# Performance work log

Hardware: AMD Instinct MI355X
Metric: run time of the kernel (lower is better)

The kernel has to match this reference:

```python
import jax, jax.numpy as jnp
import numpy as np

N, E, G = 50000, 800000, 512
DIN, H, DOUT, L = 128, 256, 128, 5
H4 = 4 * H


def _ffnn(h, W1, b1, W2, b2):
    # Linear -> exact GELU (torch default) -> Linear
    return jax.nn.gelu(h @ W1 + b1, approximate=False) @ W2 + b2


def _mean_pool(h, batch):
    s = jax.ops.segment_sum(h, batch, num_segments=G)
    c = jax.ops.segment_sum(jnp.ones((h.shape[0], 1), h.dtype), batch, num_segments=G)
    return s / jnp.maximum(c, 1.0)


def setup_inputs() -> dict:
    key = jax.random.key(0)
    ks = iter(jax.random.split(key, 64))
    w = lambda *s: jax.random.normal(next(ks), s, jnp.float32) * 0.02
    z = lambda *s: jnp.zeros(s, jnp.float32)
    inp = {
        'x': jax.random.normal(next(ks), (N, DIN), jnp.float32),
        'edge_index': jax.random.randint(next(ks), (2, E), 0, N, jnp.int32),
        'batch': jnp.sort(jax.random.randint(next(ks), (N,), 0, G, jnp.int32)),
        'pre_W1': w(DIN, H), 'pre_b1': z(H), 'pre_W2': w(H, H), 'pre_b2': z(H),
        'gin_W1': w(L, H, H), 'gin_b1': z(L, H), 'gin_W2': w(L, H, H), 'gin_b2': z(L, H),
        'ffn_W1': w(L, H, H), 'ffn_b1': z(L, H), 'ffn_W2': w(L, H, H), 'ffn_b2': z(L, H),
        'upd_W1': w(L, H, H), 'upd_b1': z(L, H), 'upd_W2': w(L, H, H4), 'upd_b2': z(L, H4),
        'prop_W1': w(L, H4, H), 'prop_b1': z(L, H), 'prop_W2': w(L, H, H), 'prop_b2': z(L, H),
        'bn_gamma': jnp.ones((L, H), jnp.float32), 'bn_beta': z(L, H),
        'vn': jax.random.normal(next(ks), (1, H4), jnp.float32),
        'post_W1': w(H, H), 'post_b1': z(H), 'post_W2': w(H, DOUT), 'post_b2': z(DOUT),
    }
    return inp


def reference(x, edge_index, batch,
              pre_W1, pre_b1, pre_W2, pre_b2,
              gin_W1, gin_b1, gin_W2, gin_b2,
              ffn_W1, ffn_b1, ffn_W2, ffn_b2,
              upd_W1, upd_b1, upd_W2, upd_b2,
              prop_W1, prop_b1, prop_W2, prop_b2,
              bn_gamma, bn_beta, vn,
              post_W1, post_b1, post_W2, post_b2):
    src, dst = edge_index[0], edge_index[1]
    h = _ffnn(x, pre_W1, pre_b1, pre_W2, pre_b2)
    for i in range(L):
        # virtual node update and propagation
        v = vn + _ffnn(_mean_pool(h, batch), upd_W1[i], upd_b1[i], upd_W2[i], upd_b2[i])  # [G, 4H]
        outvn = _ffnn(v, prop_W1[i], prop_b1[i], prop_W2[i], prop_b2[i])  # [G, H]
        # GINConv (eps=0): nn((1+eps)*h + sum_{j->i} h_j), residual
        agg = jax.ops.segment_sum(h[src], dst, num_segments=N)
        h = _ffnn(h + agg, gin_W1[i], gin_b1[i], gin_W2[i], gin_b2[i]) + h
        # BatchNorm1d (batch statistics, biased var)
        mu = jnp.mean(h, axis=0)
        var = jnp.mean((h - mu) ** 2, axis=0)
        h = (h - mu) * jax.lax.rsqrt(var + 1e-5) * bn_gamma[i] + bn_beta[i]
        # broadcast VN to nodes, FFNN with residual (dropout = identity in eval)
        h = _ffnn(outvn[batch] + h, ffn_W1[i], ffn_b1[i], ffn_W2[i], ffn_b2[i]) + h
    out = _ffnn(_mean_pool(h, batch), post_W1, post_b1, post_W2, post_b2)
    return out
```

## Files before the change

### kernel.cpp

```cpp
#include <hip/hip_runtime.h>
#include <hip/hip_bf16.h>
#include <math.h>

#define NN 50000
#define NNP 50048
#define NE 800000
#define NG 512
#define DIN 128
#define HD 256
#define DOUT 128
#define NL 5
#define H4 1024

typedef _Float16 f16x8 __attribute__((ext_vector_type(8)));
typedef _Float16 f16x4 __attribute__((ext_vector_type(4)));
typedef float f32x4 __attribute__((ext_vector_type(4)));

__device__ __forceinline__ float gelu_exact(float x) {
    return 0.5f * x * (1.0f + erff(x * 0.70710678118654752f));
}

__device__ __forceinline__ void gl_lds16(const _Float16* g, _Float16* l) {
    __builtin_amdgcn_global_load_lds(
        (const __attribute__((address_space(1))) unsigned int*)g,
        (__attribute__((address_space(3))) unsigned int*)l, 16, 0, 0);
}

__global__ void k_hist(const int* __restrict__ idx, int* __restrict__ cnt, int n) {
    int i = blockIdx.x * blockDim.x + threadIdx.x;
    if (i < n) atomicAdd(&cnt[idx[i]], 1);
}

__global__ void k_scan_small(const int* __restrict__ in, int* __restrict__ out, int n) {
    __shared__ int buf[1024];
    int t = threadIdx.x;
    int v = (t < n) ? in[t] : 0;
    buf[t] = v;
    __syncthreads();
    for (int off = 1; off < 1024; off <<= 1) {
        int x = (t >= off) ? buf[t - off] : 0;
        __syncthreads();
        buf[t] += x;
        __syncthreads();
    }
    if (t < n) out[t] = buf[t] - v;
    if (t == 1023) out[n] = buf[1023];
}

__global__ void k_scan_part(const int* __restrict__ in, int* __restrict__ bsum, int n) {
    __shared__ int buf[256];
    int i = blockIdx.x * 256 + threadIdx.x;
    buf[threadIdx.x] = (i < n) ? in[i] : 0;
    __syncthreads();
    for (int off = 128; off > 0; off >>= 1) {
        if (threadIdx.x < off) buf[threadIdx.x] += buf[threadIdx.x + off];
        __syncthreads();
    }
    if (threadIdx.x == 0) bsum[blockIdx.x] = buf[0];
}

__global__ void k_scan_mid(const int* __restrict__ bsum, int* __restrict__ bexcl, int nb,
                           int* __restrict__ out, int n) {
    __shared__ int buf[1024];
    int t = threadIdx.x;
    int v = (t < nb) ? bsum[t] : 0;
    buf[t] = v;
    __syncthreads();
    for (int off = 1; off < 1024; off <<= 1) {
        int x = (t >= off) ? buf[t - off] : 0;
        __syncthreads();
        buf[t] += x;
        __syncthreads();
    }
    if (t < nb) bexcl[t] = buf[t] - v;
    if (t == 1023) out[n] = buf[1023];
}

__global__ void k_scan_out(const int* __restrict__ in, const int* __restrict__ bexcl,
                           int* __restrict__ out, int n) {
    __shared__ int buf[256];
    int i = blockIdx.x * 256 + threadIdx.x;
    int t = threadIdx.x;
    int v = (i < n) ? in[i] : 0;
    buf[t] = v;
    __syncthreads();
    for (int off = 1; off < 256; off <<= 1) {
        int x = (t >= off) ? buf[t - off] : 0;
        __syncthreads();
        buf[t] += x;
        __syncthreads();
    }
    if (i < n) out[i] = bexcl[blockIdx.x] + buf[t] - v;
}

__global__ void k_fill_csr(const int* __restrict__ src, const int* __restrict__ dst,
                           const int* __restrict__ eoff, int* __restrict__ cursor,
                           int* __restrict__ csr, int n) {
    int e = blockIdx.x * blockDim.x + threadIdx.x;
    if (e < n) {
        int d = dst[e];
        int p = atomicAdd(&cursor[d], 1);
        csr[eoff[d] + p] = src[e];
    }
}

__global__ void k_cvt16(const float* __restrict__ in, _Float16* __restrict__ out, int n4) {
    int i = blockIdx.x * blockDim.x + threadIdx.x;
    if (i < n4) {
        float4 v = *(const float4*)&in[i * 4];
        f16x4 o = { (_Float16)v.x, (_Float16)v.y, (_Float16)v.z, (_Float16)v.w };
        *(f16x4*)&out[i * 4] = o;
    }
}

#define NWTJOBS 44
struct WtJobs {
    const float* src[NWTJOBS];
    _Float16* dst[NWTJOBS];
    short K32[NWTJOBS];
    short N32[NWTJOBS];
    short pre[NWTJOBS + 1];
};
__global__ void k_wtb(WtJobs j) {
    int bid = blockIdx.x;
    int lo = 0;
    while (j.pre[lo + 1] <= bid) ++lo;
    int tl = bid - j.pre[lo];
    int nx = j.N32[lo];
    int n0 = (tl % nx) * 32, k0 = (tl / nx) * 32;
    int K = j.K32[lo] * 32, N = nx * 32;
    const float* W = j.src[lo];
    _Float16* Wt = j.dst[lo];
    __shared__ float tile[32][33];
    for (int i = threadIdx.y; i < 32; i += 8)
        tile[i][threadIdx.x] = W[(size_t)(k0 + i) * N + n0 + threadIdx.x];
    __syncthreads();
    for (int i = threadIdx.y; i < 32; i += 8)
        Wt[(size_t)(n0 + i) * K + k0 + threadIdx.x] = (_Float16)tile[threadIdx.x][i];
}

__global__ void k_pool16(const _Float16* __restrict__ h16, const int* __restrict__ goff,
                         _Float16* __restrict__ pool) {
    int g = blockIdx.x;
    int c = threadIdx.x;
    int s = goff[g], e = goff[g + 1];
    float acc = 0.f;
    for (int r = s; r < e; ++r) acc += (float)h16[(size_t)r * HD + c];
    int cnt = e - s;
    pool[g * HD + c] = (_Float16)(acc / (float)(cnt > 0 ? cnt : 1));
}

__global__ __launch_bounds__(256) void k_agg16(const _Float16* __restrict__ h16,
                                               const int* __restrict__ eoff,
                                               const int* __restrict__ csr,
                                               _Float16* __restrict__ out) {
    int node = blockIdx.x * 4 + (threadIdx.x >> 6);
    int lane = threadIdx.x & 63;
    int half = lane >> 5, l = lane & 31;
    f16x8 mine = *(const f16x8*)&h16[(size_t)node * HD + l * 8];
    float acc[8];
#pragma unroll
    for (int q = 0; q < 8; ++q) acc[q] = half ? 0.f : (float)mine[q];
    int s = eoff[node], e = eoff[node + 1];
    for (int base = s; base < e; base += 64) {
        int myi = base + lane;
        int vidx = (myi < e) ? csr[myi] : 0;
        int cnt = min(64, e - base);
        int jj = 0;
        for (; jj + 7 < cnt; jj += 8) {
            int s0 = __shfl(vidx, jj + half);
            int s1 = __shfl(vidx, jj + 2 + half);
            int s2 = __shfl(vidx, jj + 4 + half);
            int s3 = __shfl(vidx, jj + 6 + half);
            f16x8 v0 = *(const f16x8*)&h16[(size_t)s0 * HD + l * 8];
            f16x8 v1 = *(const f16x8*)&h16[(size_t)s1 * HD + l * 8];
            f16x8 v2 = *(const f16x8*)&h16[(size_t)s2 * HD + l * 8];
            f16x8 v3 = *(const f16x8*)&h16[(size_t)s3 * HD + l * 8];
#pragma unroll
            for (int q = 0; q < 8; ++q)
                acc[q] += ((float)v0[q] + (float)v1[q]) + ((float)v2[q] + (float)v3[q]);
        }
        for (; jj + 3 < cnt; jj += 4) {
            int s0 = __shfl(vidx, jj + half);
            int s1 = __shfl(vidx, jj + 2 + half);
            f16x8 v0 = *(const f16x8*)&h16[(size_t)s0 * HD + l * 8];
            f16x8 v1 = *(const f16x8*)&h16[(size_t)s1 * HD + l * 8];
#pragma unroll
            for (int q = 0; q < 8; ++q) acc[q] += (float)v0[q] + (float)v1[q];
        }
        for (; jj < cnt; jj += 2) {
            int i0 = jj + half;
            int s0 = __shfl(vidx, i0);
            if (i0 < cnt) {
                f16x8 v0 = *(const f16x8*)&h16[(size_t)s0 * HD + l * 8];
#pragma unroll
                for (int q = 0; q < 8; ++q) acc[q] += (float)v0[q];
            }
        }
    }
#pragma unroll
    for (int q = 0; q < 8; ++q) acc[q] += __shfl_xor(acc[q], 32);
    if (!half) {
        f16x8 o;
#pragma unroll
        for (int q = 0; q < 8; ++q) o[q] = (_Float16)acc[q];
        *(f16x8*)&out[(size_t)node * HD + l * 8] = o;
    }
}

__global__ void k_bn_final(float* __restrict__ stat,
                           const float* __restrict__ gamma, const float* __restrict__ beta,
                           float* __restrict__ scale, float* __restrict__ shift) {
    int c = threadIdx.x;
    float mu = stat[c] * (1.0f / NN);
    float var = stat[HD + c] * (1.0f / NN) - mu * mu;
    float rs = rsqrtf(var + 1e-5f);
    float sc = rs * gamma[c];
    scale[c] = sc;
    shift[c] = beta[c] - mu * sc;
    stat[c] = 0.f;
    stat[HD + c] = 0.f;
}

template <bool ABN1, bool RES2, bool RESBN2, bool STATS2, int K1>
__global__ __launch_bounds__(512) void k_b2b(const _Float16* __restrict__ A16,
                                             const _Float16* __restrict__ G16,
                                             const _Float16* __restrict__ W1t,
                                             const float* __restrict__ b1,
                                             const _Float16* __restrict__ W2t,
                                             const float* __restrict__ b2,
                                             const _Float16* __restrict__ R16,
                                             const float* __restrict__ bnsc,
                                             const float* __restrict__ bnsh,
                                             const float* __restrict__ ovn,
                                             const int* __restrict__ batchv,
                                             float* __restrict__ stat,
                                             _Float16* __restrict__ C16,
                                             int M) {
    __shared__ _Float16 AC[32][64][8];
    __shared__ _Float16 Bs[3][4][256][8];
    constexpr int NT1 = K1 >> 5;
    constexpr int NSTEP = NT1 + 8;
    const int t = threadIdx.x;
    const int w = t >> 6, lane = t & 63;
    const int m0 = blockIdx.x * 64;
    const int kb = lane >> 4, fr = lane & 15, rr = lane >> 4;

    auto stageB = [&](int s) {
        const _Float16* Wt = (s < NT1) ? W1t : W2t;
        const int KB = (s < NT1) ? K1 : HD;
        const int k0 = ((s < NT1) ? s : (s - NT1)) << 5;
        const int buf = s % 3;
        int s0 = t, s1 = t + 512;
        gl_lds16(Wt + (size_t)(s0 & 255) * KB + k0 + (s0 >> 8) * 8, &Bs[buf][s0 >> 8][s0 & 255][0]);
        gl_lds16(Wt + (size_t)(s1 & 255) * KB + k0 + (s1 >> 8) * 8, &Bs[buf][s1 >> 8][s1 & 255][0]);
    };

    float b1r[2];
#pragma unroll
    for (int ni = 0; ni < 2; ++ni) b1r[ni] = b1[w * 32 + ni * 16 + fr];

    if constexpr (ABN1) {
        for (int c = t; c < K1 * 8; c += 512) {
            int kblk = c >> 6, row = c & 63;
            int b0 = batchv[min(m0 + row, M - 1)];
            const int c0 = kblk * 8;
            f16x8 g = *(const f16x8*)&G16[(size_t)(m0 + row) * HD + c0];
            f16x8 r0;
#pragma unroll
            for (int q = 0; q < 8; ++q)
                r0[q] = (_Float16)((float)g[q] * bnsc[c0 + q] + bnsh[c0 + q] +
                                   ovn[(size_t)b0 * HD + c0 + q]);
            *(f16x8*)&AC[kblk][row][0] = r0;
        }
    } else {
        for (int c = t; c < K1 * 8; c += 512) {
            int kblk = c >> 6, row = c & 63;
            gl_lds16(A16 + (size_t)(m0 + row) * K1 + kblk * 8, &AC[kblk][row][0]);
        }
    }
    stageB(0);
    stageB(1);
    asm volatile("s_waitcnt vmcnt(2) lgkmcnt(0)" ::: "memory");
    __builtin_amdgcn_s_barrier();

    f32x4 acc1[4][2];
#pragma unroll
    for (int mi = 0; mi < 4; ++mi)
#pragma unroll
        for (int ni = 0; ni < 2; ++ni) acc1[mi][ni] = (f32x4){0.f, 0.f, 0.f, 0.f};

#pragma unroll
    for (int s = 0; s < NT1; ++s) {
        if (s) {
            asm volatile("s_waitcnt vmcnt(2)" ::: "memory");
            __builtin_amdgcn_s_barrier();
        }
        f16x8 af[4], bf[2];
#pragma unroll
        for (int mi = 0; mi < 4; ++mi)
            af[mi] = *(const f16x8*)&AC[(s << 2) + kb][mi * 16 + fr][0];
#pragma unroll
        for (int ni = 0; ni < 2; ++ni)
            bf[ni] = *(const f16x8*)&Bs[s % 3][kb][w * 32 + ni * 16 + fr][0];
        stageB(s + 2);
#pragma unroll
        for (int mi = 0; mi < 4; ++mi)
#pragma unroll
            for (int ni = 0; ni < 2; ++ni)
                acc1[mi][ni] = __builtin_amdgcn_mfma_f32_16x16x32_f16(af[mi], bf[ni], acc1[mi][ni], 0, 0, 0);
    }

    asm volatile("s_waitcnt vmcnt(2)" ::: "memory");
    __builtin_amdgcn_s_barrier();
#pragma unroll
    for (int mi = 0; mi < 4; ++mi) {
#pragma unroll
        for (int reg = 0; reg < 4; ++reg) {
            int ml = mi * 16 + rr * 4 + reg;
#pragma unroll
            for (int ni = 0; ni < 2; ++ni) {
                int n = w * 32 + ni * 16 + fr;
                float v = gelu_exact(acc1[mi][ni][reg] + b1r[ni]);
                AC[n >> 3][ml][n & 7] = (_Float16)v;
            }
        }
    }
    asm volatile("s_waitcnt lgkmcnt(0)" ::: "memory");
    __builtin_amdgcn_s_barrier();

    f32x4 acc2[4][2];
#pragma unroll
    for (int mi = 0; mi < 4; ++mi)
#pragma unroll
        for (int ni = 0; ni < 2; ++ni) acc2[mi][ni] = (f32x4){0.f, 0.f, 0.f, 0.f};

#pragma unroll
    for (int s2 = 0; s2 < 8; ++s2) {
        const int s = NT1 + s2;
        if (s2) {
            if (s2 == 7) asm volatile("s_waitcnt vmcnt(0)" ::: "memory");
            else asm volatile("s_waitcnt vmcnt(2)" ::: "memory");
            __builtin_amdgcn_s_barrier();
        }
        f16x8 af[4], bf[2];
#pragma unroll
        for (int mi = 0; mi < 4; ++mi)
            af[mi] = *(const f16x8*)&AC[s2 * 4 + kb][mi * 16 + fr][0];
#pragma unroll
        for (int ni = 0; ni < 2; ++ni)
            bf[ni] = *(const f16x8*)&Bs[s % 3][kb][w * 32 + ni * 16 + fr][0];
        if (s + 2 < NSTEP) stageB(s + 2);
#pragma unroll
        for (int mi = 0; mi < 4; ++mi)
#pragma unroll
            for (int ni = 0; ni < 2; ++ni)
                acc2[mi][ni] = __builtin_amdgcn_mfma_f32_16x16x32_f16(af[mi], bf[ni], acc2[mi][ni], 0, 0, 0);
    }

    float cs[2] = {0.f, 0.f}, cq[2] = {0.f, 0.f};
#pragma unroll
    for (int mi = 0; mi < 4; ++mi) {
#pragma unroll
        for (int reg = 0; reg < 4; ++reg) {
            int m = m0 + mi * 16 + rr * 4 + reg;
            if (m < M) {
#pragma unroll
                for (int ni = 0; ni < 2; ++ni) {
                    int n = w * 32 + ni * 16 + fr;
                    float v = acc2[mi][ni][reg] + b2[n];
                    if (RES2) v += (float)R16[(size_t)m * HD + n];
                    if (RESBN2) v += (float)R16[(size_t)m * HD + n] * bnsc[n] + bnsh[n];
                    _Float16 vh = (_Float16)v;
                    C16[(size_t)m * HD + n] = vh;
                    if (STATS2) { float vr = (float)vh; cs[ni] += vr; cq[ni] += vr * vr; }
                }
            }
        }
    }
    if constexpr (STATS2) {
#pragma unroll
        for (int ni = 0; ni < 2; ++ni) {
            cs[ni] += __shfl_xor(cs[ni], 16); cs[ni] += __shfl_xor(cs[ni], 32);
            cq[ni] += __shfl_xor(cq[ni], 16); cq[ni] += __shfl_xor(cq[ni], 32);
        }
        if (lane < 16) {
#pragma unroll
            for (int ni = 0; ni < 2; ++ni) {
                int n = w * 32 + ni * 16 + lane;
                atomicAdd(&stat[n], cs[ni]);
                atomicAdd(&stat[HD + n], cq[ni]);
            }
        }
    }
}

template <bool GELU, bool BIAS2, bool O32, bool O16>
__global__ __launch_bounds__(256) void k_mgemm(const _Float16* __restrict__ A,
                                               const _Float16* __restrict__ Wt,
                                               const float* __restrict__ bias,
                                               const float* __restrict__ bias2,
                                               float* __restrict__ C32,
                                               _Float16* __restrict__ C16,
                                               int M, int N, int K) {
    __shared__ _Float16 As[2][4][64][8];
    __shared__ _Float16 Bs[2][4][128][8];
    const int t = threadIdx.x;
    const int w = t >> 6, lane = t & 63;
    const int m0 = blockIdx.y * 64, n0 = blockIdx.x * 128;
    const int kb = lane >> 4, fr = lane & 15;

    f32x4 acc[4][2];
#pragma unroll
    for (int mi = 0; mi < 4; ++mi)
#pragma unroll
        for (int ni = 0; ni < 2; ++ni) acc[mi][ni] = (f32x4){0.f, 0.f, 0.f, 0.f};

    const _Float16* gA0 = A + (size_t)(m0 + lane) * K + w * 8;
    const _Float16* gB0 = Wt + (size_t)(n0 + lane) * K + w * 8;
    const _Float16* gB1 = Wt + (size_t)(n0 + 64 + lane) * K + w * 8;

    auto stage = [&](int buf, int k0) {
        gl_lds16(gB0 + k0, &Bs[buf][w][0][0]);
        gl_lds16(gB1 + k0, &Bs[buf][w][64][0]);
        gl_lds16(gA0 + k0, &As[buf][w][0][0]);
    };

    const int nt = K >> 5;
    stage(0, 0);
    __syncthreads();
    for (int tt = 0; tt < nt; ++tt) {
        const int cur = tt & 1;
        if (tt + 1 < nt) stage(cur ^ 1, (tt + 1) << 5);
        f16x8 af[4], bf[2];
#pragma unroll
        for (int mi = 0; mi < 4; ++mi)
            af[mi] = *(const f16x8*)&As[cur][kb][mi * 16 + fr][0];
#pragma unroll
        for (int ni = 0; ni < 2; ++ni)
            bf[ni] = *(const f16x8*)&Bs[cur][kb][w * 32 + ni * 16 + fr][0];
#pragma unroll
        for (int mi = 0; mi < 4; ++mi)
#pragma unroll
            for (int ni = 0; ni < 2; ++ni)
                acc[mi][ni] = __builtin_amdgcn_mfma_f32_16x16x32_f16(af[mi], bf[ni], acc[mi][ni], 0, 0, 0);
        __syncthreads();
    }

    const int rr = lane >> 4;
#pragma unroll
    for (int mi = 0; mi < 4; ++mi) {
#pragma unroll
        for (int reg = 0; reg < 4; ++reg) {
            int m = m0 + mi * 16 + rr * 4 + reg;
            if (m < M) {
#pragma unroll
                for (int ni = 0; ni < 2; ++ni) {
                    int n = n0 + w * 32 + ni * 16 + fr;
                    float v = acc[mi][ni][reg] + bias[n];
                    if (BIAS2) v += bias2[n];
                    if (GELU) v = gelu_exact(v);
                    if (O32) C32[(size_t)m * N + n] = v;
                    if (O16) C16[(size_t)m * N + n] = (_Float16)v;
                }
            }
        }
    }
}

static inline void mg_gelu(hipStream_t st, const _Float16* A, const _Float16* Wt,
                           const float* bias, _Float16* C16, int M, int N, int K) {
    dim3 g(N / 128, (M + 63) / 64), b(256);
    k_mgemm<true, false, false, true><<<g, b, 0, st>>>(A, Wt, bias, nullptr, nullptr, C16, M, N, K);
}
static inline void mg_bias2_16(hipStream_t st, const _Float16* A, const _Float16* Wt,
                               const float* bias, const float* bias2, _Float16* C16,
                               int M, int N, int K) {
    dim3 g(N / 128, (M + 63) / 64), b(256);
    k_mgemm<false, true, false, true><<<g, b, 0, st>>>(A, Wt, bias, bias2, nullptr, C16, M, N, K);
}
static inline void mg_f32only(hipStream_t st, const _Float16* A, const _Float16* Wt,
                              const float* bias, float* C32, int M, int N, int K) {
    dim3 g(N / 128, (M + 63) / 64), b(256);
    k_mgemm<false, false, true, false><<<g, b, 0, st>>>(A, Wt, bias, nullptr, C32, nullptr, M, N, K);
}

extern "C" void kernel_launch(void* const* d_in, const int* in_sizes, int n_in,
                              void* d_out, int out_size, void* d_ws, size_t ws_size,
                              hipStream_t stream) {
    const float* x       = (const float*)d_in[0];
    const int*   ei      = (const int*)d_in[1];
    const int*   batch   = (const int*)d_in[2];
    const float* pre_W1  = (const float*)d_in[3];
    const float* pre_b1  = (const float*)d_in[4];
    const float* pre_W2  = (const float*)d_in[5];
    const float* pre_b2  = (const float*)d_in[6];
    const float* gin_W1  = (const float*)d_in[7];
    const float* gin_b1  = (const float*)d_in[8];
    const float* gin_W2  = (const float*)d_in[9];
    const float* gin_b2  = (const float*)d_in[10];
    const float* ffn_W1  = (const float*)d_in[11];
    const float* ffn_b1  = (const float*)d_in[12];
    const float* ffn_W2  = (const float*)d_in[13];
    const float* ffn_b2  = (const float*)d_in[14];
    const float* upd_W1  = (const float*)d_in[15];
    const float* upd_b1  = (const float*)d_in[16];
    const float* upd_W2  = (const float*)d_in[17];
    const float* upd_b2  = (const float*)d_in[18];
    const float* prop_W1 = (const float*)d_in[19];
    const float* prop_b1 = (const float*)d_in[20];
    const float* prop_W2 = (const float*)d_in[21];
    const float* prop_b2 = (const float*)d_in[22];
    const float* bn_gamma= (const float*)d_in[23];
    const float* bn_beta = (const float*)d_in[24];
    const float* vn      = (const float*)d_in[25];
    const float* post_W1 = (const float*)d_in[26];
    const float* post_b1 = (const float*)d_in[27];
    const float* post_W2 = (const float*)d_in[28];
    const float* post_b2 = (const float*)d_in[29];
    float* out = (float*)d_out;

    const int* e_src = ei;
    const int* e_dst = ei + NE;

    char* p = (char*)d_ws;
    auto alloc = [&](size_t bytes) -> char* {
        char* r = p;
        p += (bytes + 255) & ~(size_t)255;
        return r;
    };
    _Float16* h16    = (_Float16*)alloc((size_t)NNP * HD * 2);
    _Float16* g16    = (_Float16*)alloc((size_t)NNP * HD * 2);
    _Float16* t16a   = (_Float16*)alloc((size_t)NNP * HD * 2);
    _Float16* pool16 = (_Float16*)alloc((size_t)NG * HD * 2);
    _Float16* u16    = (_Float16*)alloc((size_t)NG * HD * 2);
    _Float16* vb16   = (_Float16*)alloc((size_t)NG * H4 * 2);
    _Float16* p16    = (_Float16*)alloc((size_t)NG * HD * 2);
    float*    outvn32= (float*)alloc((size_t)NG * HD * 4);
    float*    bnstat = (float*)alloc(2 * HD * 4);
    float*    bnscale= (float*)alloc(HD * 4);
    float*    bnshift= (float*)alloc(HD * 4);
    _Float16* preW1t = (_Float16*)alloc((size_t)HD * DIN * 2);
    _Float16* preW2t = (_Float16*)alloc((size_t)HD * HD * 2);
    _Float16* ginW1t = (_Float16*)alloc((size_t)NL * HD * HD * 2);
    _Float16* ginW2t = (_Float16*)alloc((size_t)NL * HD * HD * 2);
    _Float16* ffnW1t = (_Float16*)alloc((size_t)NL * HD * HD * 2);
    _Float16* ffnW2t = (_Float16*)alloc((size_t)NL * HD * HD * 2);
    _Float16* updW1t = (_Float16*)alloc((size_t)NL * HD * HD * 2);
    _Float16* updW2t = (_Float16*)alloc((size_t)NL * HD * H4 * 2);
    _Float16* propW1t= (_Float16*)alloc((size_t)NL * H4 * HD * 2);
    _Float16* propW2t= (_Float16*)alloc((size_t)NL * HD * HD * 2);
    _Float16* postW1t= (_Float16*)alloc((size_t)HD * HD * 2);
    _Float16* postW2t= (_Float16*)alloc((size_t)DOUT * HD * 2);
    int* gcount = (int*)alloc(NG * 4);
    int* goff   = (int*)alloc((NG + 1) * 4);
    int* deg    = (int*)alloc(NN * 4);
    int* eoff   = (int*)alloc((NN + 1) * 4);
    int* cursor = (int*)alloc(NN * 4);
    int* csr    = (int*)alloc((size_t)NE * 4);
    int* bsum   = (int*)alloc(1024 * 4);
    int* bexcl  = (int*)alloc(1024 * 4);
    _Float16* x16 = t16a;

    {
        size_t span = (size_t)((char*)(cursor + NN) - (char*)gcount);
        hipMemsetAsync(gcount, 0, span, stream);
        hipMemsetAsync(bnstat, 0, 2 * HD * 4, stream);
    }
    hipLaunchKernelGGL(k_hist, dim3((NN + 255) / 256), dim3(256), 0, stream, batch, gcount, NN);
    hipLaunchKernelGGL(k_hist, dim3((NE + 255) / 256), dim3(256), 0, stream, e_dst, deg, NE);
    hipLaunchKernelGGL(k_scan_small, dim3(1), dim3(1024), 0, stream, gcount, goff, NG);
    {
        int nbN = (NN + 255) / 256;
        hipLaunchKernelGGL(k_scan_part, dim3(nbN), dim3(256), 0, stream, deg, bsum, NN);
        hipLaunchKernelGGL(k_scan_mid, dim3(1), dim3(1024), 0, stream, bsum, bexcl, nbN, eoff, NN);
        hipLaunchKernelGGL(k_scan_out, dim3(nbN), dim3(256), 0, stream, deg, bexcl, eoff, NN);
    }
    hipLaunchKernelGGL(k_fill_csr, dim3((NE + 255) / 256), dim3(256), 0, stream, e_src, e_dst, eoff, cursor, csr, NE);

    {
        WtJobs j;
        int idx = 0, tiles = 0;
        auto add = [&](const float* s, _Float16* d, int K, int N) {
            j.src[idx] = s; j.dst[idx] = d;
            j.K32[idx] = (short)(K / 32); j.N32[idx] = (short)(N / 32);
            j.pre[idx] = (short)tiles;
            tiles += (K / 32) * (N / 32);
            ++idx;
        };
        add(pre_W1, preW1t, DIN, HD);
        add(pre_W2, preW2t, HD, HD);
        add(post_W1, postW1t, HD, HD);
        add(post_W2, postW2t, HD, DOUT);
        for (int i = 0; i < NL; ++i) {
            add(gin_W1 + (size_t)i * HD * HD, ginW1t + (size_t)i * HD * HD, HD, HD);
            add(gin_W2 + (size_t)i * HD * HD, ginW2t + (size_t)i * HD * HD, HD, HD);
            add(ffn_W1 + (size_t)i * HD * HD, ffnW1t + (size_t)i * HD * HD, HD, HD);
            add(ffn_W2 + (size_t)i * HD * HD, ffnW2t + (size_t)i * HD * HD, HD, HD);
            add(upd_W1 + (size_t)i * HD * HD, updW1t + (size_t)i * HD * HD, HD, HD);
            add(upd_W2 + (size_t)i * HD * H4, updW2t + (size_t)i * HD * H4, HD, H4);
            add(prop_W1 + (size_t)i * H4 * HD, propW1t + (size_t)i * H4 * HD, H4, HD);
            add(prop_W2 + (size_t)i * HD * HD, propW2t + (size_t)i * HD * HD, HD, HD);
        }
        j.pre[idx] = (short)tiles;
        hipLaunchKernelGGL(k_wtb, dim3(tiles), dim3(32, 8), 0, stream, j);
    }

    int n4 = NN * DIN / 4;
    hipLaunchKernelGGL(k_cvt16, dim3((n4 + 255) / 256), dim3(256), 0, stream, x, x16, n4);

    const int nb2b = NNP / 64;

    hipLaunchKernelGGL((k_b2b<false, false, false, false, DIN>), dim3(nb2b), dim3(512), 0, stream,
                       x16, nullptr, preW1t, pre_b1, preW2t, pre_b2,
                       nullptr, nullptr, nullptr, nullptr, nullptr, nullptr,
                       h16, NN);

    for (int i = 0; i < NL; ++i) {
        const _Float16* uW1 = updW1t + (size_t)i * HD * HD;
        const _Float16* uW2 = updW2t + (size_t)i * HD * H4;
        const _Float16* pW1 = propW1t + (size_t)i * H4 * HD;
        const _Float16* pW2 = propW2t + (size_t)i * HD * HD;

        hipLaunchKernelGGL(k_pool16, dim3(NG), dim3(HD), 0, stream, h16, goff, pool16);
        mg_gelu(stream, pool16, uW1, upd_b1 + (size_t)i * HD, u16, NG, HD, HD);
        mg_bias2_16(stream, u16, uW2, upd_b2 + (size_t)i * H4, vn, vb16, NG, H4, HD);
        mg_gelu(stream, vb16, pW1, prop_b1 + (size_t)i * HD, p16, NG, HD, H4);
        mg_f32only(stream, p16, pW2, prop_b2 + (size_t)i * HD, outvn32, NG, HD, HD);

        hipLaunchKernelGGL(k_agg16, dim3(NN / 4), dim3(256), 0, stream, h16, eoff, csr, t16a);
        hipLaunchKernelGGL((k_b2b<false, true, false, true, HD>), dim3(nb2b), dim3(512), 0, stream,
                           t16a, nullptr,
                           ginW1t + (size_t)i * HD * HD, gin_b1 + (size_t)i * HD,
                           ginW2t + (size_t)i * HD * HD, gin_b2 + (size_t)i * HD,
                           h16, nullptr, nullptr, nullptr, nullptr, bnstat,
                           g16, NN);

        hipLaunchKernelGGL(k_bn_final, dim3(1), dim3(HD), 0, stream, bnstat,
                           bn_gamma + (size_t)i * HD, bn_beta + (size_t)i * HD, bnscale, bnshift);

        hipLaunchKernelGGL((k_b2b<true, false, true, false, HD>), dim3(nb2b), dim3(512), 0, stream,
                           nullptr, g16,
                           ffnW1t + (size_t)i * HD * HD, ffn_b1 + (size_t)i * HD,
                           ffnW2t + (size_t)i * HD * HD, ffn_b2 + (size_t)i * HD,
                           g16, bnscale, bnshift, outvn32, batch, nullptr,
                           h16, NN);
    }

    hipLaunchKernelGGL(k_pool16, dim3(NG), dim3(HD), 0, stream, h16, goff, pool16);
    mg_gelu(stream, pool16, postW1t, post_b1, u16, NG, HD, HD);
    mg_f32only(stream, u16, postW2t, post_b2, out, NG, DOUT, HD);
}
```

Before: 1.648 ms.

## Load weight fragments directly into registers instead of staging through LDS

The fused two-layer MLP kernel stops staging weight tiles in a triple-buffered shared-memory ring via global_load_lds. Each wave now loads its own B fragments straight from global memory into registers with a three-deep register prefetch. This removes the per-k-step barriers and frees 48KB of LDS, which could raise occupancy. In exchange, each wave issues its own uncoalesced-ish global loads of weights (each weight row is read by the wave that owns those columns) and relies on L2/L1 hits rather than shared reuse.

```diff
diff --git a/kernel.cpp b/kernel.cpp
--- a/kernel.cpp
+++ b/kernel.cpp
@@ -238,27 +238,11 @@
                                              _Float16* __restrict__ C16,
                                              int M) {
     __shared__ _Float16 AC[32][64][8];
-    __shared__ _Float16 Bs[3][4][256][8];
     constexpr int NT1 = K1 >> 5;
-    constexpr int NSTEP = NT1 + 8;
     const int t = threadIdx.x;
     const int w = t >> 6, lane = t & 63;
     const int m0 = blockIdx.x * 64;
     const int kb = lane >> 4, fr = lane & 15, rr = lane >> 4;
-
-    auto stageB = [&](int s) {
-        const _Float16* Wt = (s < NT1) ? W1t : W2t;
-        const int KB = (s < NT1) ? K1 : HD;
-        const int k0 = ((s < NT1) ? s : (s - NT1)) << 5;
-        const int buf = s % 3;
-        int s0 = t, s1 = t + 512;
-        gl_lds16(Wt + (size_t)(s0 & 255) * KB + k0 + (s0 >> 8) * 8, &Bs[buf][s0 >> 8][s0 & 255][0]);
-        gl_lds16(Wt + (size_t)(s1 & 255) * KB + k0 + (s1 >> 8) * 8, &Bs[buf][s1 >> 8][s1 & 255][0]);
-    };
-
-    float b1r[2];
-#pragma unroll
-    for (int ni = 0; ni < 2; ++ni) b1r[ni] = b1[w * 32 + ni * 16 + fr];
 
     if constexpr (ABN1) {
         for (int c = t; c < K1 * 8; c += 512) {
@@ -279,10 +263,7 @@
             gl_lds16(A16 + (size_t)(m0 + row) * K1 + kblk * 8, &AC[kblk][row][0]);
         }
     }
-    stageB(0);
-    stageB(1);
-    asm volatile("s_waitcnt vmcnt(2) lgkmcnt(0)" ::: "memory");
-    __builtin_amdgcn_s_barrier();
+    __syncthreads();
 
     f32x4 acc1[4][2];
 #pragma unroll
@@ -290,29 +271,31 @@
 #pragma unroll
         for (int ni = 0; ni < 2; ++ni) acc1[mi][ni] = (f32x4){0.f, 0.f, 0.f, 0.f};
 
-#pragma unroll
-    for (int s = 0; s < NT1; ++s) {
-        if (s) {
-            asm volatile("s_waitcnt vmcnt(2)" ::: "memory");
-            __builtin_amdgcn_s_barrier();
-        }
-        f16x8 af[4], bf[2];
-#pragma unroll
-        for (int mi = 0; mi < 4; ++mi)
-            af[mi] = *(const f16x8*)&AC[(s << 2) + kb][mi * 16 + fr][0];
-#pragma unroll
-        for (int ni = 0; ni < 2; ++ni)
-            bf[ni] = *(const f16x8*)&Bs[s % 3][kb][w * 32 + ni * 16 + fr][0];
-        stageB(s + 2);
-#pragma unroll
-        for (int mi = 0; mi < 4; ++mi)
+    {
+        f16x8 bf[3][2];
+        auto loadB = [&](int s, f16x8* dst) {
 #pragma unroll
             for (int ni = 0; ni < 2; ++ni)
-                acc1[mi][ni] = __builtin_amdgcn_mfma_f32_16x16x32_f16(af[mi], bf[ni], acc1[mi][ni], 0, 0, 0);
-    }
-
-    asm volatile("s_waitcnt vmcnt(2)" ::: "memory");
-    __builtin_amdgcn_s_barrier();
+                dst[ni] = *(const f16x8*)&W1t[(size_t)(w * 32 + ni * 16 + fr) * K1 + (s << 5) + kb * 8];
+        };
+        loadB(0, bf[0]);
+        if (NT1 > 1) loadB(1, bf[1]);
+#pragma unroll
+        for (int s = 0; s < NT1; ++s) {
+            if (s + 2 < NT1) loadB(s + 2, bf[(s + 2) % 3]);
+            f16x8 af[4];
+#pragma unroll
+            for (int mi = 0; mi < 4; ++mi)
+                af[mi] = *(const f16x8*)&AC[(s << 2) + kb][mi * 16 + fr][0];
+#pragma unroll
+            for (int mi = 0; mi < 4; ++mi)
+#pragma unroll
+                for (int ni = 0; ni < 2; ++ni)
+                    acc1[mi][ni] = __builtin_amdgcn_mfma_f32_16x16x32_f16(af[mi], bf[s % 3][ni], acc1[mi][ni], 0, 0, 0);
+        }
+    }
+
+    __syncthreads();
 #pragma unroll
     for (int mi = 0; mi < 4; ++mi) {
 #pragma unroll
@@ -321,13 +304,12 @@
 #pragma unroll
             for (int ni = 0; ni < 2; ++ni) {
                 int n = w * 32 + ni * 16 + fr;
-                float v = gelu_exact(acc1[mi][ni][reg] + b1r[ni]);
+                float v = gelu_exact(acc1[mi][ni][reg] + b1[n]);
                 AC[n >> 3][ml][n & 7] = (_Float16)v;
             }
         }
     }
-    asm volatile("s_waitcnt lgkmcnt(0)" ::: "memory");
-    __builtin_amdgcn_s_barrier();
+    __syncthreads();
 
     f32x4 acc2[4][2];
 #pragma unroll
@@ -335,27 +317,28 @@
 #pragma unroll
         for (int ni = 0; ni < 2; ++ni) acc2[mi][ni] = (f32x4){0.f, 0.f, 0.f, 0.f};
 
-#pragma unroll
-    for (int s2 = 0; s2 < 8; ++s2) {
-        const int s = NT1 + s2;
-        if (s2) {
-            if (s2 == 7) asm volatile("s_waitcnt vmcnt(0)" ::: "memory");
-            else asm volatile("s_waitcnt vmcnt(2)" ::: "memory");
-            __builtin_amdgcn_s_barrier();
-        }
-        f16x8 af[4], bf[2];
-#pragma unroll
-        for (int mi = 0; mi < 4; ++mi)
-            af[mi] = *(const f16x8*)&AC[s2 * 4 + kb][mi * 16 + fr][0];
-#pragma unroll
-        for (int ni = 0; ni < 2; ++ni)
-            bf[ni] = *(const f16x8*)&Bs[s % 3][kb][w * 32 + ni * 16 + fr][0];
-        if (s + 2 < NSTEP) stageB(s + 2);
-#pragma unroll
-        for (int mi = 0; mi < 4; ++mi)
+    {
+        f16x8 bf[3][2];
+        auto loadB = [&](int s, f16x8* dst) {
 #pragma unroll
             for (int ni = 0; ni < 2; ++ni)
-                acc2[mi][ni] = __builtin_amdgcn_mfma_f32_16x16x32_f16(af[mi], bf[ni], acc2[mi][ni], 0, 0, 0);
+                dst[ni] = *(const f16x8*)&W2t[(size_t)(w * 32 + ni * 16 + fr) * HD + (s << 5) + kb * 8];
+        };
+        loadB(0, bf[0]);
+        loadB(1, bf[1]);
+#pragma unroll
+        for (int s = 0; s < 8; ++s) {
+            if (s + 2 < 8) loadB(s + 2, bf[(s + 2) % 3]);
+            f16x8 af[4];
+#pragma unroll
+            for (int mi = 0; mi < 4; ++mi)
+                af[mi] = *(const f16x8*)&AC[s * 4 + kb][mi * 16 + fr][0];
+#pragma unroll
+            for (int mi = 0; mi < 4; ++mi)
+#pragma unroll
+                for (int ni = 0; ni < 2; ++ni)
+                    acc2[mi][ni] = __builtin_amdgcn_mfma_f32_16x16x32_f16(af[mi], bf[s % 3][ni], acc2[mi][ni], 0, 0, 0);
+        }
     }
 
     float cs[2] = {0.f, 0.f}, cq[2] = {0.f, 0.f};
```

New measurement: 1.639 ms. Within noise of the previous version (-0.5%).
